# Optimization experiments

Hardware: AMD Instinct MI355X
Metric: run time of the kernel (lower is better)

Reference implementation:

```python
import jax, jax.numpy as jnp
import numpy as np

HID = 256      # hidden_size
NH = 4         # num_heads
DH = HID // NH # att_size
N_MOLS = 2048
MAX_LEN = 128  # max bonds per molecule (static pad length)
LN_EPS = 1e-5


def setup_inputs() -> dict:
    rng = np.random.default_rng(0)
    sizes = rng.integers(32, MAX_LEN + 1, size=N_MOLS).astype(np.int32)
    starts = (1 + np.concatenate([[0], np.cumsum(sizes)[:-1]])).astype(np.int32)
    total = int(1 + sizes.sum())  # row 0 is the chemprop padding bond

    key = jax.random.key(0)
    ks = jax.random.split(key, 5)
    s = HID ** -0.5
    message = jax.random.normal(ks[0], (total, HID), jnp.float32)
    Wq = jax.random.normal(ks[1], (HID, HID), jnp.float32) * s
    Wk = jax.random.normal(ks[2], (HID, HID), jnp.float32) * s
    Wv = jax.random.normal(ks[3], (HID, HID), jnp.float32) * s
    Wo = jax.random.normal(ks[4], (HID, HID), jnp.float32) * s
    bo = jnp.zeros((HID,), jnp.float32)
    gamma = jnp.ones((HID,), jnp.float32)
    beta = jnp.zeros((HID,), jnp.float32)
    return dict(message=message, Wq=Wq, Wk=Wk, Wv=Wv, Wo=Wo, bo=bo,
                gamma=gamma, beta=beta,
                b_starts=jnp.asarray(starts), b_sizes=jnp.asarray(sizes))


def reference(message, Wq, Wk, Wv, Wo, bo, gamma, beta, b_starts, b_sizes):
    total = message.shape[0]
    # Padded gather: [M, L, HID] block view of the ragged segments.
    ar = jnp.arange(MAX_LEN)
    pos = b_starts[:, None] + ar[None, :]              # [M, L]
    mask = ar[None, :] < b_sizes[:, None]              # [M, L] valid bonds
    idx = jnp.where(mask, pos, 0)
    x = message[idx]                                   # [M, L, HID]

    # QKV (torch Linear: y = x @ W.T), split heads.
    q = jnp.einsum('mlf,gf->mlg', x, Wq).reshape(N_MOLS, MAX_LEN, NH, DH)
    k = jnp.einsum('mlf,gf->mlg', x, Wk).reshape(N_MOLS, MAX_LEN, NH, DH)
    v = jnp.einsum('mlf,gf->mlg', x, Wv).reshape(N_MOLS, MAX_LEN, NH, DH)

    scale = DH ** -0.5
    scores = jnp.einsum('mqnd,mknd->mnqk', q, k) * scale   # [M, NH, L, L]
    neg = jnp.finfo(scores.dtype).min
    scores = jnp.where(mask[:, None, None, :], scores, neg)
    attn = jax.nn.softmax(scores, axis=-1)

    o = jnp.einsum('mnqk,mknd->mqnd', attn, v)             # [M, L, NH, DH]
    o = jax.nn.relu(o).reshape(N_MOLS, MAX_LEN, HID)       # act_func = ReLU; dropout = identity (eval)
    o = jnp.einsum('mlf,gf->mlg', o, Wo) + bo              # output projection

    # LayerNorm over hidden dim (per-molecule as in original, but LN is per-row anyway)
    mu = jnp.mean(o, axis=-1, keepdims=True)
    var = jnp.mean(jnp.square(o - mu), axis=-1, keepdims=True)
    o = (o - mu) * jax.lax.rsqrt(var + LN_EPS) * gamma + beta

    # Scatter back; row 0 stays zero (cached_zero_vector). Invalid pads -> OOB index, dropped.
    tgt = jnp.where(mask, pos, total)
    out = jnp.zeros_like(message)
    out = out.at[tgt.reshape(-1)].set(o.reshape(-1, HID), mode='drop')
    return out
```

## Files before the change

kernel.cpp:

```cpp
#include <hip/hip_runtime.h>
#include <hip/hip_bf16.h>

#define HID 256
#define NH 4
#define DH 64

typedef __attribute__((ext_vector_type(8))) short bf16x8;
typedef __attribute__((ext_vector_type(4))) short bf16x4;
typedef __attribute__((ext_vector_type(4))) float f32x4;

#define MFMA16(a, b, c) __builtin_amdgcn_mfma_f32_16x16x32_bf16((a), (b), (c), 0, 0, 0)

__device__ __forceinline__ f32x4 mfma16k(bf16x4 a, bf16x4 b, f32x4 c) {
  asm("v_mfma_f32_16x16x16_bf16 %0, %1, %2, %0" : "+v"(c) : "v"(a), "v"(b));
  return c;
}

#define LQK 72
#define LVT 136

__device__ __forceinline__ short f2bf(float f) {
  unsigned u = __float_as_uint(f);
  unsigned r = (u + 0x7fffu + ((u >> 16) & 1u)) >> 16;
  return (short)r;
}

__device__ __forceinline__ bf16x8 ld_cvt8(const float* p) {
  float4 a = *(const float4*)p;
  float4 b = *(const float4*)(p + 4);
  bf16x8 r;
  r[0] = f2bf(a.x); r[1] = f2bf(a.y); r[2] = f2bf(a.z); r[3] = f2bf(a.w);
  r[4] = f2bf(b.x); r[5] = f2bf(b.y); r[6] = f2bf(b.z); r[7] = f2bf(b.w);
  return r;
}

__global__ __launch_bounds__(256) void cvt_w_kernel(
    const float* __restrict__ Wq, const float* __restrict__ Wk,
    const float* __restrict__ Wv, const float* __restrict__ Wo,
    short* __restrict__ Wb)
{
  const int id   = blockIdx.x * 256 + threadIdx.x;
  const int lane = id & 63;
  const int ks   = (id >> 6) & 7;
  const int nt   = (id >> 9) & 3;
  const int h    = (id >> 11) & 3;
  const int mat  = id >> 13;
  const float* src[4] = {Wq, Wk, Wv, Wo};
  const int row = h * 64 + nt * 16 + (lane & 15);
  const int col = ks * 32 + (lane >> 4) * 8;
  *(bf16x8*)(Wb + (size_t)id * 8) = ld_cvt8(src[mat] + row * HID + col);
}

__global__ __launch_bounds__(256) void cvt_msg_kernel(
    const float* __restrict__ src, short* __restrict__ dst, int n8)
{
  int i = blockIdx.x * 256 + threadIdx.x;
  const int stride = gridDim.x * 256;
  for (; i < n8; i += stride)
    *(bf16x8*)(dst + (size_t)i * 8) = ld_cvt8(src + (size_t)i * 8);
}

template<bool XB>
__global__ __launch_bounds__(256, 4) void attn_kernel(
    const void* __restrict__ xsrc, const short* __restrict__ Wb,
    const int* __restrict__ starts, const int* __restrict__ sizes,
    short* __restrict__ O)
{
  __shared__ __align__(16) short K_s[128 * LQK];
  __shared__ __align__(16) short V_t[DH * LVT];

  const int b = blockIdx.x;
  int mol, head;
  if ((gridDim.x & 31) == 0) { mol = (b & 7) + ((b >> 5) << 3); head = (b >> 3) & 3; }
  else                       { mol = b >> 2;  head = b & 3; }

  const int L     = sizes[mol];
  const int start = starts[mol];
  const int Mt    = (L + 15) >> 4;

  const int tid  = threadIdx.x;
  const int wave = tid >> 6;
  const int lane = tid & 63;
  const int c = lane & 15;
  const int g = lane >> 4;

  bf16x4 qb[2][4];

  const bf16x8 zf = {0, 0, 0, 0, 0, 0, 0, 0};
  #pragma unroll
  for (int i = 0; i < 2; i++) {
    const int mt = wave + 4 * i;
    if (mt >= Mt) break;

    bf16x8 a[8];
    {
      int rl = mt * 16 + c;
      bool v = rl < L;
      if constexpr (XB) {
        const short* xp = (const short*)xsrc + (size_t)(start + (v ? rl : 0)) * HID + g * 8;
        #pragma unroll
        for (int ks = 0; ks < 8; ks++) { bf16x8 t = *(const bf16x8*)(xp + ks * 32); a[ks] = v ? t : zf; }
      } else {
        const float* xp = (const float*)xsrc + (size_t)(start + (v ? rl : 0)) * HID + g * 8;
        #pragma unroll
        for (int ks = 0; ks < 8; ks++) { bf16x8 t = ld_cvt8(xp + ks * 32); a[ks] = v ? t : zf; }
      }
    }

    #pragma unroll
    for (int nt = 0; nt < 12; nt++) {
      const short* Wp = Wb + ((size_t)(((nt >> 2) * 4 + head) * 4 + (nt & 3)) << 12) + lane * 8;
      bf16x8 bw[8];
      #pragma unroll
      for (int ks = 0; ks < 8; ks++) bw[ks] = *(const bf16x8*)(Wp + ks * 512);

      f32x4 acc = {0.f, 0.f, 0.f, 0.f};
      if (nt < 4) {
        #pragma unroll
        for (int ks = 0; ks < 8; ks++) acc = MFMA16(bw[ks], a[ks], acc);
        #pragma unroll
        for (int r = 0; r < 4; r++) qb[i][nt][r] = f2bf(acc[r] * 0.125f);
      } else {
        #pragma unroll
        for (int ks = 0; ks < 8; ks++) acc = MFMA16(a[ks], bw[ks], acc);
        #pragma unroll
        for (int r = 0; r < 4; r++) {
          short val = f2bf(acc[r]);
          int row = mt * 16 + g * 4 + r;
          if (nt < 8) K_s[row * LQK + (nt - 4) * 16 + c] = val;
          else        V_t[((nt - 8) * 16 + c) * LVT + row] = val;
        }
      }
    }
  }
  __syncthreads();

  #pragma unroll
  for (int i = 0; i < 2; i++) {
    const int mt = wave + 4 * i;
    if (mt >= Mt) continue;

    float sv[8][4];
    #pragma unroll
    for (int nt = 0; nt < 8; nt++) {
      if (nt < Mt) {
        f32x4 acc = {0.f, 0.f, 0.f, 0.f};
        #pragma unroll
        for (int ks = 0; ks < 4; ks++) {
          bf16x4 kb = *(const bf16x4*)&K_s[(nt * 16 + c) * LQK + ks * 16 + g * 4];
          acc = mfma16k(kb, qb[i][ks], acc);
        }
        sv[nt][0] = acc[0]; sv[nt][1] = acc[1]; sv[nt][2] = acc[2]; sv[nt][3] = acc[3];
      }
    }

    float mr = -3.0e38f;
    #pragma unroll
    for (int nt = 0; nt < 8; nt++) {
      if (nt < Mt) {
        #pragma unroll
        for (int r = 0; r < 4; r++) {
          int key = nt * 16 + g * 4 + r;
          float v = (key < L) ? sv[nt][r] : -3.0e38f;
          sv[nt][r] = v;
          mr = fmaxf(mr, v);
        }
      }
    }
    mr = fmaxf(mr, __shfl_xor(mr, 16));
    mr = fmaxf(mr, __shfl_xor(mr, 32));
    float sum = 0.f;
    #pragma unroll
    for (int nt = 0; nt < 8; nt++) {
      if (nt < Mt) {
        #pragma unroll
        for (int r = 0; r < 4; r++) {
          float e = (sv[nt][r] > -1.0e37f) ? __expf(sv[nt][r] - mr) : 0.f;
          sv[nt][r] = e;
          sum += e;
        }
      }
    }
    sum += __shfl_xor(sum, 16);
    sum += __shfl_xor(sum, 32);
    float inv = 1.f / sum;

    bf16x4 pa[8];
    #pragma unroll
    for (int nt = 0; nt < 8; nt++) {
      if (nt < Mt) {
        #pragma unroll
        for (int r = 0; r < 4; r++) pa[nt][r] = f2bf(sv[nt][r] * inv);
      }
    }

    #pragma unroll
    for (int nt2 = 0; nt2 < 4; nt2++) {
      f32x4 acc = {0.f, 0.f, 0.f, 0.f};
      #pragma unroll
      for (int nt = 0; nt < 8; nt++) {
        if (nt < Mt) {
          bf16x4 vb = *(const bf16x4*)&V_t[(nt2 * 16 + c) * LVT + nt * 16 + g * 4];
          acc = mfma16k(pa[nt], vb, acc);
        }
      }
      #pragma unroll
      for (int r = 0; r < 4; r++) {
        int rl = mt * 16 + g * 4 + r;
        if (rl < L)
          O[(size_t)(start + rl) * HID + head * 64 + nt2 * 16 + c] =
              f2bf(fmaxf(acc[r], 0.f));
      }
    }
  }
}

__global__ __launch_bounds__(256) void proj_ln_kernel(
    const short* __restrict__ Ob, const short* __restrict__ Wb,
    const float* __restrict__ bo, const float* __restrict__ gamma,
    const float* __restrict__ beta, float* __restrict__ out, int total)
{
  __shared__ __align__(16) float o_s[32 * 260];
  short* ob_s = (short*)o_s;
  const int base = blockIdx.x * 32;
  const int tid  = threadIdx.x;
  const int wave = tid >> 6;
  const int lane = tid & 63;
  const int c = lane & 15, g = lane >> 4;

  #pragma unroll
  for (int t = 0; t < 4; t++) {
    int q = tid + t * 256;
    int row = q >> 5, cc = q & 31;
    int grow = base + row; if (grow >= total) grow = total - 1;
    *(bf16x8*)&ob_s[row * 264 + cc * 8] = *(const bf16x8*)(Ob + (size_t)grow * HID + cc * 8);
  }
  __syncthreads();

  bf16x8 a[2][8];
  #pragma unroll
  for (int i = 0; i < 2; i++)
    #pragma unroll
    for (int ks = 0; ks < 8; ks++)
      a[i][ks] = *(const bf16x8*)&ob_s[(i * 16 + c) * 264 + ks * 32 + g * 8];
  __syncthreads();

  #pragma unroll
  for (int nt = 0; nt < 4; nt++) {
    const short* Wp = Wb + ((size_t)((12 + wave) * 4 + nt) << 12) + lane * 8;
    bf16x8 b[8];
    #pragma unroll
    for (int ks = 0; ks < 8; ks++) b[ks] = *(const bf16x8*)(Wp + ks * 512);
    #pragma unroll
    for (int i = 0; i < 2; i++) {
      f32x4 acc = {0.f, 0.f, 0.f, 0.f};
      #pragma unroll
      for (int ks = 0; ks < 8; ks++) acc = MFMA16(a[i][ks], b[ks], acc);
      #pragma unroll
      for (int r = 0; r < 4; r++)
        o_s[(i * 16 + g * 4 + r) * 260 + wave * 64 + nt * 16 + c] = acc[r];
    }
  }
  __syncthreads();

  float4 bo4 = *(const float4*)(bo + lane * 4);
  float4 g4  = *(const float4*)(gamma + lane * 4);
  float4 b4  = *(const float4*)(beta + lane * 4);
  #pragma unroll
  for (int r8 = 0; r8 < 8; r8++) {
    int rl = wave * 8 + r8;
    float4 o = *(const float4*)&o_s[rl * 260 + lane * 4];
    o.x += bo4.x; o.y += bo4.y; o.z += bo4.z; o.w += bo4.w;
    float s  = o.x + o.y + o.z + o.w;
    float ss = o.x * o.x + o.y * o.y + o.z * o.z + o.w * o.w;
    #pragma unroll
    for (int off = 32; off; off >>= 1) { s += __shfl_xor(s, off); ss += __shfl_xor(ss, off); }
    float mu  = s * (1.f / HID);
    float var = ss * (1.f / HID) - mu * mu;
    float inv = rsqrtf(var + 1e-5f);
    int row = base + rl;
    if (row < total) {
      float4 res;
      res.x = (o.x - mu) * inv * g4.x + b4.x;
      res.y = (o.y - mu) * inv * g4.y + b4.y;
      res.z = (o.z - mu) * inv * g4.z + b4.z;
      res.w = (o.w - mu) * inv * g4.w + b4.w;
      if (row == 0) res = make_float4(0.f, 0.f, 0.f, 0.f);
      *(float4*)(out + (size_t)row * HID + lane * 4) = res;
    }
  }
}

extern "C" void kernel_launch(void* const* d_in, const int* in_sizes, int n_in,
                              void* d_out, int out_size, void* d_ws, size_t ws_size,
                              hipStream_t stream) {
  const float* msg   = (const float*)d_in[0];
  const float* Wq    = (const float*)d_in[1];
  const float* Wk    = (const float*)d_in[2];
  const float* Wv    = (const float*)d_in[3];
  const float* Wo    = (const float*)d_in[4];
  const float* bo    = (const float*)d_in[5];
  const float* gamma = (const float*)d_in[6];
  const float* beta  = (const float*)d_in[7];
  const int* starts  = (const int*)d_in[8];
  const int* sizes   = (const int*)d_in[9];

  const int nmols = in_sizes[8];
  const int total = in_sizes[0] / HID;

  short* O  = (short*)d_ws;
  short* Wb = O + (size_t)total * HID;
  short* Xb = Wb + 4 * HID * HID;

  size_t need = ((size_t)total * HID * 2 + 4 * HID * HID) * sizeof(short);
  const bool use_xb = ws_size >= need;

  cvt_w_kernel<<<128, 256, 0, stream>>>(Wq, Wk, Wv, Wo, Wb);
  if (use_xb) {
    int n8 = total * (HID / 8);
    int gsz = (n8 + 255) / 256; if (gsz > 2048) gsz = 2048;
    cvt_msg_kernel<<<gsz, 256, 0, stream>>>(msg, Xb, n8);
    attn_kernel<true><<<nmols * NH, 256, 0, stream>>>(Xb, Wb, starts, sizes, O);
  } else {
    attn_kernel<false><<<nmols * NH, 256, 0, stream>>>(msg, Wb, starts, sizes, O);
  }
  proj_ln_kernel<<<(total + 31) / 32, 256, 0, stream>>>(
      O, Wb, bo, gamma, beta, (float*)d_out, total);
}
```

Baseline: 596.5 us.

## Keep projection accumulators in registers and do LayerNorm via cross-wave partial sums

The output-projection plus LayerNorm kernel now handles 64 rows per block instead of 32, which halves how often each block reloads the Wo weight tiles. It no longer writes the fp32 projection result to shared memory and reads it back for LayerNorm. Each wave reduces row sums and sums of squares over its 64 columns with lane shuffles, then combines the four waves' partials through a small shared array. The final normalized values are written straight from the MFMA accumulator layout, so each store covers only 16 contiguous floats per row fragment rather than full float4-per-lane rows. This adds register pressure (64 accumulator floats) and reads A fragments from shared memory inside the nt loop.

```diff
diff --git a/kernel.cpp b/kernel.cpp
--- a/kernel.cpp
+++ b/kernel.cpp
@@ -18,6 +18,7 @@
 
 #define LQK 72
 #define LVT 136
+#define LOB 272
 
 __device__ __forceinline__ short f2bf(float f) {
   unsigned u = __float_as_uint(f);
@@ -220,73 +221,90 @@
     const float* __restrict__ bo, const float* __restrict__ gamma,
     const float* __restrict__ beta, float* __restrict__ out, int total)
 {
-  __shared__ __align__(16) float o_s[32 * 260];
-  short* ob_s = (short*)o_s;
-  const int base = blockIdx.x * 32;
+  __shared__ __align__(16) short ob_s[64 * LOB];
+  __shared__ float red[64][4][2];
+  const int base = blockIdx.x * 64;
   const int tid  = threadIdx.x;
   const int wave = tid >> 6;
   const int lane = tid & 63;
   const int c = lane & 15, g = lane >> 4;
 
   #pragma unroll
-  for (int t = 0; t < 4; t++) {
+  for (int t = 0; t < 8; t++) {
     int q = tid + t * 256;
     int row = q >> 5, cc = q & 31;
     int grow = base + row; if (grow >= total) grow = total - 1;
-    *(bf16x8*)&ob_s[row * 264 + cc * 8] = *(const bf16x8*)(Ob + (size_t)grow * HID + cc * 8);
+    *(bf16x8*)&ob_s[row * LOB + cc * 8] = *(const bf16x8*)(Ob + (size_t)grow * HID + cc * 8);
   }
   __syncthreads();
 
-  bf16x8 a[2][8];
-  #pragma unroll
-  for (int i = 0; i < 2; i++)
-    #pragma unroll
-    for (int ks = 0; ks < 8; ks++)
-      a[i][ks] = *(const bf16x8*)&ob_s[(i * 16 + c) * 264 + ks * 32 + g * 8];
-  __syncthreads();
-
+  f32x4 acc[4][4];
   #pragma unroll
   for (int nt = 0; nt < 4; nt++) {
     const short* Wp = Wb + ((size_t)((12 + wave) * 4 + nt) << 12) + lane * 8;
-    bf16x8 b[8];
-    #pragma unroll
-    for (int ks = 0; ks < 8; ks++) b[ks] = *(const bf16x8*)(Wp + ks * 512);
-    #pragma unroll
-    for (int i = 0; i < 2; i++) {
-      f32x4 acc = {0.f, 0.f, 0.f, 0.f};
-      #pragma unroll
-      for (int ks = 0; ks < 8; ks++) acc = MFMA16(a[i][ks], b[ks], acc);
-      #pragma unroll
-      for (int r = 0; r < 4; r++)
-        o_s[(i * 16 + g * 4 + r) * 260 + wave * 64 + nt * 16 + c] = acc[r];
+    bf16x8 bw[8];
+    #pragma unroll
+    for (int ks = 0; ks < 8; ks++) bw[ks] = *(const bf16x8*)(Wp + ks * 512);
+    #pragma unroll
+    for (int i = 0; i < 4; i++) {
+      f32x4 a4 = {0.f, 0.f, 0.f, 0.f};
+      #pragma unroll
+      for (int ks = 0; ks < 8; ks++) {
+        bf16x8 a = *(const bf16x8*)&ob_s[(i * 16 + c) * LOB + ks * 32 + g * 8];
+        a4 = MFMA16(a, bw[ks], a4);
+      }
+      acc[nt][i] = a4;
+    }
+  }
+
+  float boc[4], gc[4], bc[4];
+  #pragma unroll
+  for (int nt = 0; nt < 4; nt++) {
+    int col = wave * 64 + nt * 16 + c;
+    boc[nt] = bo[col]; gc[nt] = gamma[col]; bc[nt] = beta[col];
+  }
+  #pragma unroll
+  for (int i = 0; i < 4; i++) {
+    #pragma unroll
+    for (int r = 0; r < 4; r++) {
+      float s = 0.f, ss = 0.f;
+      #pragma unroll
+      for (int nt = 0; nt < 4; nt++) {
+        float v = acc[nt][i][r] + boc[nt];
+        acc[nt][i][r] = v;
+        s += v; ss += v * v;
+      }
+      s += __shfl_xor(s, 1);  ss += __shfl_xor(ss, 1);
+      s += __shfl_xor(s, 2);  ss += __shfl_xor(ss, 2);
+      s += __shfl_xor(s, 4);  ss += __shfl_xor(ss, 4);
+      s += __shfl_xor(s, 8);  ss += __shfl_xor(ss, 8);
+      if (c == 0) {
+        int row = i * 16 + g * 4 + r;
+        red[row][wave][0] = s;
+        red[row][wave][1] = ss;
+      }
     }
   }
   __syncthreads();
 
-  float4 bo4 = *(const float4*)(bo + lane * 4);
-  float4 g4  = *(const float4*)(gamma + lane * 4);
-  float4 b4  = *(const float4*)(beta + lane * 4);
-  #pragma unroll
-  for (int r8 = 0; r8 < 8; r8++) {
-    int rl = wave * 8 + r8;
-    float4 o = *(const float4*)&o_s[rl * 260 + lane * 4];
-    o.x += bo4.x; o.y += bo4.y; o.z += bo4.z; o.w += bo4.w;
-    float s  = o.x + o.y + o.z + o.w;
-    float ss = o.x * o.x + o.y * o.y + o.z * o.z + o.w * o.w;
-    #pragma unroll
-    for (int off = 32; off; off >>= 1) { s += __shfl_xor(s, off); ss += __shfl_xor(ss, off); }
-    float mu  = s * (1.f / HID);
-    float var = ss * (1.f / HID) - mu * mu;
-    float inv = rsqrtf(var + 1e-5f);
-    int row = base + rl;
-    if (row < total) {
-      float4 res;
-      res.x = (o.x - mu) * inv * g4.x + b4.x;
-      res.y = (o.y - mu) * inv * g4.y + b4.y;
-      res.z = (o.z - mu) * inv * g4.z + b4.z;
-      res.w = (o.w - mu) * inv * g4.w + b4.w;
-      if (row == 0) res = make_float4(0.f, 0.f, 0.f, 0.f);
-      *(float4*)(out + (size_t)row * HID + lane * 4) = res;
+  #pragma unroll
+  for (int i = 0; i < 4; i++) {
+    #pragma unroll
+    for (int r = 0; r < 4; r++) {
+      int row = i * 16 + g * 4 + r;
+      int grow = base + row;
+      if (grow < total) {
+        float s  = red[row][0][0] + red[row][1][0] + red[row][2][0] + red[row][3][0];
+        float ss = red[row][0][1] + red[row][1][1] + red[row][2][1] + red[row][3][1];
+        float mu  = s * (1.f / HID);
+        float inv = rsqrtf(ss * (1.f / HID) - mu * mu + 1e-5f);
+        #pragma unroll
+        for (int nt = 0; nt < 4; nt++) {
+          float v = (grow == 0) ? 0.f
+                    : (acc[nt][i][r] - mu) * inv * gc[nt] + bc[nt];
+          out[(size_t)grow * HID + wave * 64 + nt * 16 + c] = v;
+        }
+      }
     }
   }
 }
@@ -324,6 +342,6 @@
   } else {
     attn_kernel<false><<<nmols * NH, 256, 0, stream>>>(msg, Wb, starts, sizes, O);
   }
-  proj_ln_kernel<<<(total + 31) / 32, 256, 0, stream>>>(
+  proj_ln_kernel<<<(total + 63) / 64, 256, 0, stream>>>(
       O, Wb, bo, gamma, beta, (float*)d_out, total);
 }
```

New measurement: 608.9 us. 2.1% more time.
